# Optimization experiments

Hardware: AMD Instinct MI355X
Metric: run time of the kernel (lower is better)

The kernel has to match this reference:

```python
import jax, jax.numpy as jnp
import numpy as np


def setup_inputs() -> dict:
    key = jax.random.key(0)
    k1, k2, k3 = jax.random.split(key, 3)
    B, C, H, W, F, K = 8, 32, 64, 64, 64, 3
    x = jax.random.normal(k1, (B, C, H, W), dtype=jnp.float32)
    # per-weight rational (safe Pade [5/4]) coefficients: one activation per (f, a, b, c)
    num_coef = jax.random.normal(k2, (F, K, K, C, 6), dtype=jnp.float32) * 0.1
    den_coef = jax.random.normal(k3, (F, K, K, C, 4), dtype=jnp.float32) * 0.1
    return {"x": x, "num_coef": num_coef, "den_coef": den_coef}


def _rational(x, an, bd):
    """Safe Pade rational: P(x)/(1+|x*(b1+x*(b2+x*(b3+x*b4)))|).
    x: [B,H,W,K,K,C]; an: [K,K,C,6]; bd: [K,K,C,4] (broadcast over B,H,W)."""
    num = an[..., 5]
    for i in (4, 3, 2, 1, 0):  # Horner, ascending coeff order a0..a5
        num = num * x + an[..., i]
    q = bd[..., 3]
    for i in (2, 1, 0):
        q = q * x + bd[..., i]
    den = 1.0 + jnp.abs(q * x)
    return num / den


def reference(x, num_coef, den_coef):
    B, C, H, W = x.shape
    F, K = num_coef.shape[0], num_coef.shape[1]
    p = (K - 1) // 2
    xp = jnp.pad(x, ((0, 0), (0, 0), (p, p), (p, p)))  # zero pad H,W
    xp = jnp.transpose(xp, (0, 2, 3, 1))  # [B, H+2p, W+2p, C]
    # im2col patches: [B, H, W, K, K, C]
    patches = jnp.stack(
        [jnp.stack([xp[:, a:a + H, b:b + W, :] for b in range(K)], axis=3)
         for a in range(K)], axis=3)

    def per_filter(coefs):
        an, bd = coefs  # [K,K,C,6], [K,K,C,4]
        y = _rational(patches, an, bd)  # [B,H,W,K,K,C]
        return jnp.sum(y, axis=(3, 4, 5))  # [B,H,W]

    out = jax.lax.map(per_filter, (num_coef, den_coef))  # [F,B,H,W]
    return jnp.transpose(out, (1, 0, 2, 3))  # [B,F,H,W]
```

## Files before the change

kernel.cpp:

```cpp
#include <hip/hip_runtime.h>


typedef int   iv4  __attribute__((ext_vector_type(4)));
typedef short s8v  __attribute__((ext_vector_type(8)));
typedef float f16v __attribute__((ext_vector_type(16)));

#define Bb 8
#define Cc 32
#define Hh 64
#define Ww 64
#define Ff 64
#define PW 66
#define PPLANE (PW * PW)
#define NELEM  (Bb * Cc * PPLANE)
#define NTAP   288
#define PWBLK  (NELEM / 256)

static __device__ __forceinline__ unsigned short f2bf(float f) {
    unsigned u = __builtin_bit_cast(unsigned, f);
    u += 0x7fffu + ((u >> 16) & 1u);
    return (unsigned short)(u >> 16);
}
static __device__ __forceinline__ float bf2f(unsigned short h) {
    unsigned u = ((unsigned)h) << 16;
    return __builtin_bit_cast(float, u);
}
static __device__ __forceinline__ int pack2(unsigned short a, unsigned short b) {
    return (int)((unsigned)a | ((unsigned)b << 16));
}

static __device__ __forceinline__ void mfma2_v(s8v ad, s8v an, s8v b, f16v zf,
                                               f16v& Dd, f16v& Dn) {
    asm("s_nop 1\n\t"
        "v_mfma_f32_32x32x16_bf16 %0, %2, %4, %5\n\t"
        "v_mfma_f32_32x32x16_bf16 %1, %3, %4, %5\n\t"
        "s_nop 7\n\t"
        "s_nop 7\n\t"
        "s_nop 7"
        : "=&v"(Dd), "=&v"(Dn)
        : "v"(ad), "v"(an), "v"(b), "v"(zf));
}

__global__ __launch_bounds__(256) void prep_kernel(
    const float* __restrict__ x,
    const float* __restrict__ ncf, const float* __restrict__ dcf,
    iv4* __restrict__ pw, iv4* __restrict__ ac)
{
    if ((int)blockIdx.x < PWBLK) {
        int idx = (int)blockIdx.x * 256 + (int)threadIdx.x;
        int wp = idx % PW;
        int r1 = idx / PW;
        int hp = r1 % PW;
        int pl = r1 / PW;
        float v = 0.0f;
        if (hp >= 1 && hp <= Hh && wp >= 1 && wp <= Ww)
            v = x[((size_t)pl * Hh + (hp - 1)) * Ww + (wp - 1)];
        float p2 = v * v, p3 = p2 * v, p4 = p2 * p2, p5 = p4 * v;
        float pv[6] = {1.0f, v, p2, p3, p4, p5};
        unsigned short hi[6], lo[6];
#pragma unroll
        for (int e = 0; e < 6; ++e) {
            hi[e] = f2bf(pv[e]);
            lo[e] = f2bf(pv[e] - bf2f(hi[e]));
        }
        iv4 r0, r1v;
        r0.x  = pack2(hi[0], hi[1]); r0.y  = pack2(hi[2], hi[3]);
        r0.z  = pack2(hi[4], hi[5]); r0.w  = pack2(lo[1], lo[2]);
        r1v.x = pack2(lo[3], lo[4]); r1v.y = pack2(lo[5], hi[1]);
        r1v.z = pack2(hi[2], hi[3]); r1v.w = pack2(hi[4], hi[5]);
        pw[idx]         = r0;
        pw[NELEM + idx] = r1v;
    } else {
        int idx = ((int)blockIdx.x - PWBLK) * 256 + (int)threadIdx.x;
        int l = idx & 63, tile = (idx >> 6) & 3, t = idx >> 8;
        int m = l & 31, g = l >> 5;
        float cv[6];
        if (tile < 2) {
            int f = tile * 32 + m;
            const float* s = ncf + ((size_t)f * NTAP + t) * 6;
            cv[0] = s[0]; cv[1] = s[1]; cv[2] = s[2];
            cv[3] = s[3]; cv[4] = s[4]; cv[5] = s[5];
        } else {
            int f = (tile - 2) * 32 + m;
            const float* s = dcf + ((size_t)f * NTAP + t) * 4;
            cv[0] = 0.0f; cv[1] = s[0]; cv[2] = s[1];
            cv[3] = s[2]; cv[4] = s[3]; cv[5] = 0.0f;
        }
        unsigned short chi[6], clo[6];
#pragma unroll
        for (int e = 0; e < 6; ++e) {
            chi[e] = f2bf(cv[e]);
            clo[e] = f2bf(cv[e] - bf2f(chi[e]));
        }
        iv4 o;
        if (g == 0) {
            o.x = pack2(chi[0], chi[1]); o.y = pack2(chi[2], chi[3]);
            o.z = pack2(chi[4], chi[5]); o.w = pack2(chi[1], chi[2]);
        } else {
            o.x = pack2(chi[3], chi[4]); o.y = pack2(chi[5], clo[1]);
            o.z = pack2(clo[2], clo[3]); o.w = pack2(clo[4], clo[5]);
        }
        ac[idx] = o;
    }
}

__global__ __launch_bounds__(512, 4) void kan_mfma_kernel(
    const iv4* __restrict__ pw, const iv4* __restrict__ ac,
    float* __restrict__ out)
{
    const int tid = threadIdx.x;
    const int l = tid & 63, v = tid >> 6, ln = l & 31, g = l >> 5;
    const int p = v & 1, q = v >> 1;
    const int gb = (int)blockIdx.x;
    const int wh = gb & 1, h = (gb >> 1) & 63, bb = gb >> 7;
    const int w0 = wh << 5;

    __shared__ float red[4][2][64][16];

    f16v acc, zf;
#pragma unroll
    for (int r = 0; r < 16; ++r) { acc[r] = 0.0f; zf[r] = 0.0f; }

    const iv4* __restrict__ pwg = pw + (size_t)g * NELEM;

    const int t0 = q * 72, tEnd = t0 + 72;

    {
    }
    int k2 = t0 >> 5;
    int dy = k2 / 3, dx = k2 - dy * 3;
    int elem = ((bb * Cc + (t0 & 31)) * PW + (h + dy)) * PW + (w0 + ln + dx);
    const iv4* apl = ac + (size_t)t0 * 256 + p * 64 + l;
    iv4 blc = pwg[elem];
    iv4 Anc = apl[0], Adc = apl[128];

#pragma unroll 1
    for (int t = t0; t < tEnd; ++t) {
        const int tn = t + 1;
        const int tl = (tn < tEnd) ? tn : t;
        int elemn;
        if (tl == t) {
            elemn = elem;
        } else if ((tl & 31) == 0) {
            const int k2n = tl >> 5;
            const int dyn = k2n / 3, dxn = k2n - dyn * 3;
            elemn = (bb * Cc * PW + (h + dyn)) * PW + (w0 + ln + dxn);
        } else {
            elemn = elem + PPLANE;
        }
        const iv4* apn = apl + (size_t)(tl - t) * 256;
        iv4 bln = pwg[elemn];
        iv4 Ann = apn[0], Adn = apn[128];

        f16v Dd, Dn;
        mfma2_v(__builtin_bit_cast(s8v, Adc), __builtin_bit_cast(s8v, Anc),
                __builtin_bit_cast(s8v, blc), zf, Dd, Dn);

#pragma unroll
        for (int r = 0; r < 16; ++r) {
            float dd = 1.0f + __builtin_fabsf(Dd[r]);
            float rc = __builtin_amdgcn_rcpf(dd);
            acc[r] = __builtin_fmaf(Dn[r], rc, acc[r]);
        }

        elem = elemn; apl = apn;
        blc = bln; Anc = Ann; Adc = Adn;
    }

#pragma unroll
    for (int r = 0; r < 16; ++r)
        red[q][p][l][r ^ ((l >> 1) & 15)] = acc[r];
    __syncthreads();

    const int p2 = v & 1;
#pragma unroll
    for (int jj = 0; jj < 4; ++jj) {
        int r = (v >> 1) * 4 + jj;
        int rs = r ^ ((l >> 1) & 15);
        float s = red[0][p2][l][rs] + red[1][p2][l][rs]
                + red[2][p2][l][rs] + red[3][p2][l][rs];
        int f = p2 * 32 + (r & 3) + ((r >> 2) << 3) + ((l >> 5) << 2);
        out[(((size_t)bb * Ff + f) * Hh + h) * Ww + w0 + ln] = s;
    }
}

extern "C" void kernel_launch(void* const* d_in, const int* in_sizes, int n_in,
                              void* d_out, int out_size, void* d_ws, size_t ws_size,
                              hipStream_t stream) {
    const float* x   = (const float*)d_in[0];
    const float* ncf = (const float*)d_in[1];
    const float* dcf = (const float*)d_in[2];
    float* out = (float*)d_out;

    iv4* pw = (iv4*)d_ws;
    iv4* ac = pw + 2 * NELEM;

    prep_kernel<<<PWBLK + NTAP, 256, 0, stream>>>(x, ncf, dcf, pw, ac);
    kan_mfma_kernel<<<1024, 512, 0, stream>>>(pw, ac, out);
}
```

Before: 165.4 us.

## Process two taps per iteration with combined reciprocal and compiler-scheduled MFMA

Unrolls the tap loop by two, issuing four MFMAs per iteration through the builtin instead of inline asm padded with s_nop stalls. The two rational terms share one reciprocal via n0/d0 + n1/d1 = (n0*d1 + n1*d0)/(d0*d1), halving the rcp count. The explicit software prefetch of next-iteration operands is dropped, so load latency hiding now depends on the compiler and on occupancy. The product of denominators could lose some precision or overflow for large values.

After: 163.9 us. Within noise of the previous version (-0.9%).

```diff
diff --git a/kernel.cpp b/kernel.cpp
--- a/kernel.cpp
+++ b/kernel.cpp
@@ -27,18 +27,6 @@
 }
 static __device__ __forceinline__ int pack2(unsigned short a, unsigned short b) {
     return (int)((unsigned)a | ((unsigned)b << 16));
-}
-
-static __device__ __forceinline__ void mfma2_v(s8v ad, s8v an, s8v b, f16v zf,
-                                               f16v& Dd, f16v& Dn) {
-    asm("s_nop 1\n\t"
-        "v_mfma_f32_32x32x16_bf16 %0, %2, %4, %5\n\t"
-        "v_mfma_f32_32x32x16_bf16 %1, %3, %4, %5\n\t"
-        "s_nop 7\n\t"
-        "s_nop 7\n\t"
-        "s_nop 7"
-        : "=&v"(Dd), "=&v"(Dn)
-        : "v"(ad), "v"(an), "v"(b), "v"(zf));
 }
 
 __global__ __launch_bounds__(256) void prep_kernel(
@@ -122,49 +110,54 @@
     for (int r = 0; r < 16; ++r) { acc[r] = 0.0f; zf[r] = 0.0f; }
 
     const iv4* __restrict__ pwg = pw + (size_t)g * NELEM;
-
-    const int t0 = q * 72, tEnd = t0 + 72;
+    const int t0 = q * 72;
 
     {
     }
-    int k2 = t0 >> 5;
-    int dy = k2 / 3, dx = k2 - dy * 3;
-    int elem = ((bb * Cc + (t0 & 31)) * PW + (h + dy)) * PW + (w0 + ln + dx);
+    int k20 = t0 >> 5;
+    int dy0 = k20 / 3, dx0 = k20 - 3 * dy0;
+    int elemBase = ((bb * Cc + (t0 & 31)) * PW + (h + dy0)) * PW + (w0 + ln + dx0);
     const iv4* apl = ac + (size_t)t0 * 256 + p * 64 + l;
-    iv4 blc = pwg[elem];
-    iv4 Anc = apl[0], Adc = apl[128];
 
 #pragma unroll 1
-    for (int t = t0; t < tEnd; ++t) {
-        const int tn = t + 1;
-        const int tl = (tn < tEnd) ? tn : t;
-        int elemn;
-        if (tl == t) {
-            elemn = elem;
-        } else if ((tl & 31) == 0) {
-            const int k2n = tl >> 5;
-            const int dyn = k2n / 3, dxn = k2n - dyn * 3;
-            elemn = (bb * Cc * PW + (h + dyn)) * PW + (w0 + ln + dxn);
-        } else {
-            elemn = elem + PPLANE;
+    for (int j = 0; j < 36; ++j) {
+        const int tp = t0 + 2 * j;
+        if (j > 0) {
+            if ((tp & 31) == 0) {
+                const int k2 = tp >> 5;
+                const int dy = k2 / 3, dx = k2 - 3 * dy;
+                elemBase = (bb * Cc * PW + (h + dy)) * PW + (w0 + ln + dx);
+            } else {
+                elemBase += 2 * PPLANE;
+            }
         }
-        const iv4* apn = apl + (size_t)(tl - t) * 256;
-        iv4 bln = pwg[elemn];
-        iv4 Ann = apn[0], Adn = apn[128];
 
-        f16v Dd, Dn;
-        mfma2_v(__builtin_bit_cast(s8v, Adc), __builtin_bit_cast(s8v, Anc),
-                __builtin_bit_cast(s8v, blc), zf, Dd, Dn);
+        iv4 B0  = pwg[elemBase];
+        iv4 B1  = pwg[elemBase + PPLANE];
+        iv4 An0 = apl[0],   Ad0 = apl[128];
+        iv4 An1 = apl[256], Ad1 = apl[384];
+        apl += 512;
+
+        s8v b0 = __builtin_bit_cast(s8v, B0);
+        s8v b1 = __builtin_bit_cast(s8v, B1);
+
+        f16v Dn0 = __builtin_amdgcn_mfma_f32_32x32x16_bf16(
+            __builtin_bit_cast(s8v, An0), b0, zf, 0, 0, 0);
+        f16v Dd0 = __builtin_amdgcn_mfma_f32_32x32x16_bf16(
+            __builtin_bit_cast(s8v, Ad0), b0, zf, 0, 0, 0);
+        f16v Dn1 = __builtin_amdgcn_mfma_f32_32x32x16_bf16(
+            __builtin_bit_cast(s8v, An1), b1, zf, 0, 0, 0);
+        f16v Dd1 = __builtin_amdgcn_mfma_f32_32x32x16_bf16(
+            __builtin_bit_cast(s8v, Ad1), b1, zf, 0, 0, 0);
 
 #pragma unroll
         for (int r = 0; r < 16; ++r) {
-            float dd = 1.0f + __builtin_fabsf(Dd[r]);
-            float rc = __builtin_amdgcn_rcpf(dd);
-            acc[r] = __builtin_fmaf(Dn[r], rc, acc[r]);
+            float da = 1.0f + __builtin_fabsf(Dd0[r]);
+            float db = 1.0f + __builtin_fabsf(Dd1[r]);
+            float nn = __builtin_fmaf(Dn0[r], db, Dn1[r] * da);
+            float rc = __builtin_amdgcn_rcpf(da * db);
+            acc[r] = __builtin_fmaf(nn, rc, acc[r]);
         }
-
-        elem = elemn; apl = apn;
-        blc = bln; Anc = Ann; Adc = Adn;
     }
 
 #pragma unroll
```
